# Kernel tuning notes

Measured on AMD Instinct MI355X. Metric: run time of the kernel, lower is better.

## Reference

```python
import jax, jax.numpy as jnp
import numpy as np
from math import sqrt

V, D, H, HD, L, F, P, NL = 32000, 768, 12, 64, 12, 3072, 2048, 2
B, S = 8, 1024
EPS = 1e-5


def setup_inputs() -> dict:
    key = jax.random.key(0)
    ks = jax.random.split(key, 12)
    n = lambda k, sh: (jax.random.normal(k, sh, jnp.float32) * 0.02)
    return {
        'tokens': jax.random.randint(ks[0], (B, S), 0, V, dtype=jnp.int32),
        'tok_emb': n(ks[1], (V, D)),
        'pos_emb': n(ks[2], (P, D)),
        'emb_ln_s': jnp.ones((D,), jnp.float32), 'emb_ln_b': jnp.zeros((D,), jnp.float32),
        'Wq': n(ks[3], (L, H, D, HD)), 'bq': jnp.zeros((L, H, HD), jnp.float32),
        'Wk': n(ks[4], (L, H, D, HD)), 'bk': jnp.zeros((L, H, HD), jnp.float32),
        'Wv': n(ks[5], (L, H, D, HD)), 'bv': jnp.zeros((L, H, HD), jnp.float32),
        'Wo': n(ks[6], (L, D, D)), 'bo': jnp.zeros((L, D), jnp.float32),
        'ln1_s': jnp.ones((L, D), jnp.float32), 'ln1_b': jnp.zeros((L, D), jnp.float32),
        'ln2_s': jnp.ones((L, D), jnp.float32), 'ln2_b': jnp.zeros((L, D), jnp.float32),
        'W1': n(ks[7], (L, D, F)), 'b1': jnp.zeros((L, F), jnp.float32),
        'W2': n(ks[8], (L, F, D)), 'b2': jnp.zeros((L, D), jnp.float32),
        'Wc': n(ks[9], (D, NL)), 'bc': jnp.zeros((NL,), jnp.float32),
    }


def _ln(x, s, b):
    m = jnp.mean(x, -1, keepdims=True)
    v = jnp.mean((x - m) ** 2, -1, keepdims=True)
    return (x - m) * jax.lax.rsqrt(v + EPS) * s + b


def reference(tokens, tok_emb, pos_emb, emb_ln_s, emb_ln_b,
              Wq, bq, Wk, bk, Wv, bv, Wo, bo,
              ln1_s, ln1_b, ln2_s, ln2_b, W1, b1, W2, b2, Wc, bc):
    b, s = tokens.shape
    # embeddings (dropout is eval-mode identity)
    x = tok_emb[tokens] + pos_emb[:s][None, :, :]          # [b, s, D]
    x = _ln(x, emb_ln_s, emb_ln_b)
    scale = 1.0 / sqrt(HD)
    for l in range(L):
        xn = _ln(x, ln1_s[l], ln1_b[l])
        q = jnp.einsum('bsd,hdk->bhsk', xn, Wq[l]) + bq[l][:, None, :]
        k = jnp.einsum('bsd,hdk->bhsk', xn, Wk[l]) + bk[l][:, None, :]
        v = jnp.einsum('bsd,hdk->bhsk', xn, Wv[l]) + bv[l][:, None, :]
        scores = jnp.einsum('bhsk,bhtk->bhst', q, k) * scale   # [b,H,s,s]
        w = jax.nn.softmax(scores, axis=-1)
        o = jnp.einsum('bhst,bhtk->bhsk', w, v)                # [b,H,s,HD]
        o = o.transpose(0, 2, 1, 3).reshape(b, s, D)           # concat heads
        x = x + o @ Wo[l] + bo[l]
        xn = _ln(x, ln2_s[l], ln2_b[l])
        h = jax.nn.gelu(xn @ W1[l] + b1[l], approximate=False)
        x = x + h @ W2[l] + b2[l]
    # CLS token -> classifier (dropout identity)
    return x[:, 0, :] @ Wc + bc                                # [b, NL]
```

## Files before the change

### kernel.cpp

```cpp
#include <hip/hip_runtime.h>
#include <hip/hip_bf16.h>
#include <math.h>

#define B_   8
#define S_   1024
#define D_   768
#define H_   12
#define HD_  64
#define L_   12
#define F_   3072
#define NTOK 8192

typedef __bf16 bf16x8 __attribute__((ext_vector_type(8)));
typedef float  f32x4  __attribute__((ext_vector_type(4)));
typedef unsigned short u16;

static __device__ __forceinline__ unsigned short f2bf_bits(float f) {
    __hip_bfloat16 h = __float2bfloat16(f);
    return __builtin_bit_cast(unsigned short, h);
}
static __device__ __forceinline__ float bf2f(unsigned short u) {
    unsigned int t = ((unsigned int)u) << 16;
    return __builtin_bit_cast(float, t);
}
static __device__ __forceinline__ void gload16(const void* g, void* l) {
    __builtin_amdgcn_global_load_lds(
        (__attribute__((address_space(1))) void*)g,
        (__attribute__((address_space(3))) void*)l, 16, 0, 0);
}

__global__ __launch_bounds__(256)
void prep_layer_kernel(const float* __restrict__ Wq, const float* __restrict__ Wk,
                       const float* __restrict__ Wv, const float* __restrict__ Wo,
                       const float* __restrict__ W1, const float* __restrict__ W2,
                       int l, __hip_bfloat16* __restrict__ wbuf)
{
    const int id = blockIdx.x;
    const float* src; __hip_bfloat16* dst;
    int R, C, r0, c0;
    if (id < 432) {
        int dtile = id % 12, t = id / 12;
        int which = t / 12, h = t % 12;
        src = (which == 0 ? Wq : which == 1 ? Wk : Wv) + (size_t)(l*12 + h) * 768 * 64;
        dst = wbuf + (size_t)(which*768 + h*64) * 768;
        R = 768; C = 64; r0 = dtile * 64; c0 = 0;
    } else if (id < 576) {
        int t = id - 432;
        src = Wo + (size_t)l * 768 * 768;
        dst = wbuf + 1769472;
        R = 768; C = 768; r0 = (t / 12) * 64; c0 = (t % 12) * 64;
    } else if (id < 1152) {
        int t = id - 576;
        src = W1 + (size_t)l * 768 * 3072;
        dst = wbuf + 2359296;
        R = 768; C = 3072; r0 = (t % 12) * 64; c0 = (t / 12) * 64;
    } else {
        int t = id - 1152;
        src = W2 + (size_t)l * 3072 * 768;
        dst = wbuf + 4718592;
        R = 3072; C = 768; r0 = (t / 12) * 64; c0 = (t % 12) * 64;
    }
    __shared__ float tile[64][65];
    for (int i = threadIdx.x; i < 4096; i += 256) {
        int rr = i >> 6, cc = i & 63;
        tile[rr][cc] = src[(size_t)(r0 + rr) * C + (c0 + cc)];
    }
    __syncthreads();
    for (int i = threadIdx.x; i < 4096; i += 256) {
        int cc = i >> 6, rr = i & 63;
        dst[(size_t)(c0 + cc) * R + (r0 + rr)] = __float2bfloat16(tile[rr][cc]);
    }
}

__global__ __launch_bounds__(256)
void prep_bqkv_kernel(const float* __restrict__ bq, const float* __restrict__ bk,
                      const float* __restrict__ bv, float* __restrict__ bqkv)
{
    int i = blockIdx.x * 256 + threadIdx.x;
    int l = i / 2304, c = i % 2304;
    int which = c / 768, hk = c % 768;
    const float* src = which == 0 ? bq : which == 1 ? bk : bv;
    bqkv[i] = src[l*768 + hk];
}

__global__ __launch_bounds__(256)
void embed_ln_kernel(const int* __restrict__ tokens, const float* __restrict__ tok_emb,
                     const float* __restrict__ pos_emb, const float* __restrict__ gam,
                     const float* __restrict__ bet, float* __restrict__ x)
{
    const int row  = blockIdx.x*4 + (threadIdx.x >> 6);
    const int lane = threadIdx.x & 63;
    const int s    = row & (S_-1);
    const int tok  = tokens[row];
    const float* te = tok_emb + (size_t)tok * D_;
    const float* pe = pos_emb + (size_t)s   * D_;
    float v[12]; float s1 = 0.f, s2 = 0.f;
#pragma unroll
    for (int c = 0; c < 3; ++c) {
        const int base = c*256 + lane*4;
        float4 a = *(const float4*)(te + base);
        float4 p = *(const float4*)(pe + base);
        float t0 = a.x+p.x, t1 = a.y+p.y, t2 = a.z+p.z, t3 = a.w+p.w;
        v[c*4+0]=t0; v[c*4+1]=t1; v[c*4+2]=t2; v[c*4+3]=t3;
        s1 += t0+t1+t2+t3;
        s2 += t0*t0 + t1*t1 + t2*t2 + t3*t3;
    }
#pragma unroll
    for (int off = 32; off > 0; off >>= 1) { s1 += __shfl_xor(s1, off); s2 += __shfl_xor(s2, off); }
    const float mean = s1 * (1.f/768.f);
    const float rstd = rsqrtf(s2*(1.f/768.f) - mean*mean + 1e-5f);
    float* xr = x + (size_t)row * D_;
#pragma unroll
    for (int c = 0; c < 3; ++c) {
        const int base = c*256 + lane*4;
        float4 g = *(const float4*)(gam + base);
        float4 bb = *(const float4*)(bet + base);
        float4 o;
        o.x = (v[c*4+0]-mean)*rstd*g.x + bb.x;
        o.y = (v[c*4+1]-mean)*rstd*g.y + bb.y;
        o.z = (v[c*4+2]-mean)*rstd*g.z + bb.z;
        o.w = (v[c*4+3]-mean)*rstd*g.w + bb.w;
        *(float4*)(xr + base) = o;
    }
}

__global__ __launch_bounds__(256)
void ln_kernel(const float* __restrict__ xin, const float* __restrict__ gam,
               const float* __restrict__ bet, __hip_bfloat16* __restrict__ out)
{
    const int row  = blockIdx.x*4 + (threadIdx.x >> 6);
    const int lane = threadIdx.x & 63;
    const float* xr = xin + (size_t)row * D_;
    float v[12]; float s1 = 0.f, s2 = 0.f;
#pragma unroll
    for (int c = 0; c < 3; ++c) {
        float4 t = *(const float4*)(xr + c*256 + lane*4);
        v[c*4+0]=t.x; v[c*4+1]=t.y; v[c*4+2]=t.z; v[c*4+3]=t.w;
        s1 += t.x+t.y+t.z+t.w;
        s2 += t.x*t.x + t.y*t.y + t.z*t.z + t.w*t.w;
    }
#pragma unroll
    for (int off = 32; off > 0; off >>= 1) { s1 += __shfl_xor(s1, off); s2 += __shfl_xor(s2, off); }
    const float mean = s1 * (1.f/768.f);
    const float rstd = rsqrtf(s2*(1.f/768.f) - mean*mean + 1e-5f);
    unsigned short* op = (unsigned short*)out + (size_t)row * D_;
#pragma unroll
    for (int c = 0; c < 3; ++c) {
        const int base = c*256 + lane*4;
        float4 g = *(const float4*)(gam + base);
        float4 bb = *(const float4*)(bet + base);
        ushort4 pk;
        pk.x = f2bf_bits((v[c*4+0]-mean)*rstd*g.x + bb.x);
        pk.y = f2bf_bits((v[c*4+1]-mean)*rstd*g.y + bb.y);
        pk.z = f2bf_bits((v[c*4+2]-mean)*rstd*g.z + bb.z);
        pk.w = f2bf_bits((v[c*4+3]-mean)*rstd*g.w + bb.w);
        *(ushort4*)(op + base) = pk;
    }
}

template<int EPI>
__global__ __launch_bounds__(256)
void gemm_kernel(const __hip_bfloat16* __restrict__ A,
                 const __hip_bfloat16* __restrict__ Bt,
                 const float* __restrict__ bias,
                 __hip_bfloat16* __restrict__ outb,
                 __hip_bfloat16* __restrict__ outv,
                 float* __restrict__ outf,
                 int M, int N, int K, int nTiles)
{
    __shared__ __hip_bfloat16 As[128*64];
    __shared__ __hip_bfloat16 Bs[128*64];

    const int tid  = threadIdx.x;
    const int lane = tid & 63;
    const int wid  = tid >> 6;

    const int nwg   = gridDim.x;
    const int chunk = nwg >> 3;
    const int bid   = blockIdx.x;
    const int swz   = (bid & 7) * chunk + (bid >> 3);
    const int m0 = (swz / nTiles) * 128;
    const int n0 = (swz % nTiles) * 128;

    const int srow = wid*32 + (lane >> 3);
    const int scol = ((lane & 7) ^ (srow & 7)) * 8;
    const __hip_bfloat16* aSrc = A  + (size_t)(m0 + srow) * K + scol;
    const __hip_bfloat16* bSrc = Bt + (size_t)(n0 + srow) * K + scol;
    char* aDst = (char*)As + wid*4096 + lane*16;
    char* bDst = (char*)Bs + wid*4096 + lane*16;

    f32x4 acc[4][4] = {};
    const int wm = wid >> 1, wn = wid & 1;
    const int cl = lane & 15, hi = lane >> 4;

    for (int kt = 0; kt < K; kt += 64) {
        __syncthreads();
#pragma unroll
        for (int i = 0; i < 4; ++i)
            gload16(aSrc + kt + (size_t)i*8*K, aDst + i*1024);
#pragma unroll
        for (int i = 0; i < 4; ++i)
            gload16(bSrc + kt + (size_t)i*8*K, bDst + i*1024);
        __syncthreads();

#pragma unroll
        for (int kk = 0; kk < 2; ++kk) {
            bf16x8 af[4], bfr[4];
#pragma unroll
            for (int m = 0; m < 4; ++m) {
                int row  = wm*64 + m*16 + cl;
                int slot = ((kk<<2) + hi) ^ (row & 7);
                af[m] = *(const bf16x8*)((const char*)As + row*128 + slot*16);
            }
#pragma unroll
            for (int n = 0; n < 4; ++n) {
                int row  = wn*64 + n*16 + cl;
                int slot = ((kk<<2) + hi) ^ (row & 7);
                bfr[n] = *(const bf16x8*)((const char*)Bs + row*128 + slot*16);
            }
#pragma unroll
            for (int m = 0; m < 4; ++m)
#pragma unroll
                for (int n = 0; n < 4; ++n)
                    acc[m][n] = __builtin_amdgcn_mfma_f32_16x16x32_bf16(af[m], bfr[n], acc[m][n], 0, 0, 0);
        }
    }

    const int rowBase = m0 + wm*64;
    const int colBase = n0 + wn*64;

    if constexpr (EPI == 0) {
        if (n0 < 1536) {
#pragma unroll
            for (int n = 0; n < 4; ++n) {
                const int col = colBase + n*16 + cl;
                const float bv = bias[col];
#pragma unroll
                for (int m = 0; m < 4; ++m) {
#pragma unroll
                    for (int i = 0; i < 4; ++i) {
                        const int row = rowBase + m*16 + hi*4 + i;
                        outb[(size_t)row*1536 + col] = __float2bfloat16(acc[m][n][i] + bv);
                    }
                }
            }
        } else {
#pragma unroll
            for (int n = 0; n < 4; ++n) {
                const int col = colBase + n*16 + cl;
                const float bv = bias[col];
                const int hd = col - 1536;
                u16* vrow = (u16*)outv + (size_t)hd * 1024;
#pragma unroll
                for (int m = 0; m < 4; ++m) {
                    const int row0 = rowBase + m*16 + hi*4;
                    const int b = row0 >> 10, s0 = row0 & 1023;
                    ushort4 pk;
                    pk.x = f2bf_bits(acc[m][n][0] + bv);
                    pk.y = f2bf_bits(acc[m][n][1] + bv);
                    pk.z = f2bf_bits(acc[m][n][2] + bv);
                    pk.w = f2bf_bits(acc[m][n][3] + bv);
                    *(ushort4*)(vrow + (size_t)b*12*64*1024 + s0) = pk;
                }
            }
        }
    } else {
#pragma unroll
        for (int n = 0; n < 4; ++n) {
            const int col = colBase + n*16 + cl;
            const float bv = bias[col];
#pragma unroll
            for (int m = 0; m < 4; ++m) {
#pragma unroll
                for (int i = 0; i < 4; ++i) {
                    const int row = rowBase + m*16 + hi*4 + i;
                    float v = acc[m][n][i] + bv;
                    if constexpr (EPI == 1) {
                        float g = 0.5f * v * (1.0f + erff(v * 0.70710678118f));
                        outb[(size_t)row*N + col] = __float2bfloat16(g);
                    } else {
                        outf[(size_t)row*N + col] += v;
                    }
                }
            }
        }
    }
    (void)M;
}

__global__ __launch_bounds__(256)
void attn_kernel(const __hip_bfloat16* __restrict__ qkb, const __hip_bfloat16* __restrict__ vtb,
                 __hip_bfloat16* __restrict__ attno)
{
    __shared__ __align__(16) char Ks[2][8192];
    __shared__ __align__(16) char Vs[2][8192];
    __shared__ __align__(16) char Ps[8192];

    const u16* qk = (const u16*)qkb;
    const u16* vt = (const u16*)vtb;
    const int nwg = gridDim.x, bid = blockIdx.x, chunk = nwg >> 3;
    const int swz = (bid & 7) * chunk + (bid >> 3);
    const int bh = swz >> 4, qb = swz & 15;
    const int b = bh / H_, h = bh % H_;
    const int tid = threadIdx.x;
    const int lane = tid & 63, wid = tid >> 6;
    const int cl = lane & 15, hi = lane >> 4;
    const size_t browq = (size_t)(b*S_ + qb*64);

    bf16x8 qf[2];
    {
        const u16* qp = qk + (browq + wid*16 + cl)*1536 + h*64;
        qf[0] = *(const bf16x8*)(qp + hi*8);
        qf[1] = *(const bf16x8*)(qp + 32 + hi*8);
    }

    const int lrow = lane >> 3;
    const int scol = ((lane & 7) ^ lrow) * 8;
    const u16* kbase = qk + ((size_t)b*S_ + wid*16 + lrow)*1536 + 768 + h*64 + scol;
    const u16* vbase = vt + (((size_t)(b*H_ + h))*64 + wid*16 + lrow)*1024 + scol;
    const int ldst = wid*2048 + lane*16;

    f32x4 acc_o[4] = {};
    float m_run = -1e30f;
    float l_part[4] = {0.f, 0.f, 0.f, 0.f};
    char* pbase = Ps + wid*2048;

    {
        gload16(kbase,                 Ks[0] + ldst);
        gload16(kbase + (size_t)8*1536, Ks[0] + ldst + 1024);
        gload16(vbase,                 Vs[0] + ldst);
        gload16(vbase + 8*1024,        Vs[0] + ldst + 1024);
    }

    for (int t = 0; t < 16; ++t) {
        __syncthreads();
        if (t < 15) {
            const int nb = (t+1) & 1;
            const u16* kn = kbase + (size_t)(t+1)*64*1536;
            const u16* vn = vbase + (t+1)*64;
            gload16(kn,                  Ks[nb] + ldst);
            gload16(kn + (size_t)8*1536, Ks[nb] + ldst + 1024);
            gload16(vn,                  Vs[nb] + ldst);
            gload16(vn + 8*1024,         Vs[nb] + ldst + 1024);
        }
        const char* ks = Ks[t & 1];
        const char* vs = Vs[t & 1];

        f32x4 sc[4] = {};
#pragma unroll
        for (int kk = 0; kk < 2; ++kk) {
            bf16x8 kf[4];
#pragma unroll
            for (int n = 0; n < 4; ++n) {
                const int row = n*16 + cl;
                kf[n] = *(const bf16x8*)(ks + row*128 + (((kk*4 + hi) ^ (cl & 7)) << 4));
            }
#pragma unroll
            for (int n = 0; n < 4; ++n)
                sc[n] = __builtin_amdgcn_mfma_f32_16x16x32_bf16(qf[kk], kf[n], sc[n], 0, 0, 0);
        }

#pragma unroll
        for (int n = 0; n < 4; ++n)
#pragma unroll
            for (int i = 0; i < 4; ++i)
                sc[n][i] *= 0.125f;

        float gmax = sc[0][0];
#pragma unroll
        for (int n = 0; n < 4; ++n)
#pragma unroll
            for (int i = 0; i < 4; ++i)
                gmax = fmaxf(gmax, sc[n][i]);
        gmax = fmaxf(gmax, __shfl_xor(gmax, 1));
        gmax = fmaxf(gmax, __shfl_xor(gmax, 2));
        gmax = fmaxf(gmax, __shfl_xor(gmax, 4));
        gmax = fmaxf(gmax, __shfl_xor(gmax, 8));
        if (gmax > m_run + 4.0f) {
            const float corr = __expf(m_run - gmax);
            m_run = gmax;
#pragma unroll
            for (int i = 0; i < 4; ++i) l_part[i] *= corr;
#pragma unroll
            for (int nd = 0; nd < 4; ++nd)
#pragma unroll
                for (int i = 0; i < 4; ++i)
                    acc_o[nd][i] *= corr;
        }

#pragma unroll
        for (int n = 0; n < 4; ++n) {
#pragma unroll
            for (int i = 0; i < 4; ++i) {
                const float e = __expf(sc[n][i] - m_run);
                l_part[i] += e;
                const int q = hi*4 + i;
                const int slot = (n*2 + (cl >> 3)) ^ (q & 7);
                *(u16*)(pbase + q*128 + slot*16 + (cl & 7)*2) = f2bf_bits(e);
            }
        }

        asm volatile("s_waitcnt lgkmcnt(0)" ::: "memory");
        __builtin_amdgcn_sched_barrier(0);

#pragma unroll
        for (int kk = 0; kk < 2; ++kk) {
            const bf16x8 pf = *(const bf16x8*)(pbase + cl*128 + (((kk*4 + hi) ^ (cl & 7)) << 4));
            bf16x8 vf[4];
#pragma unroll
            for (int nd = 0; nd < 4; ++nd) {
                const int d = nd*16 + cl;
                vf[nd] = *(const bf16x8*)(vs + d*128 + (((kk*4 + hi) ^ (d & 7)) << 4));
            }
#pragma unroll
            for (int nd = 0; nd < 4; ++nd)
                acc_o[nd] = __builtin_amdgcn_mfma_f32_16x16x32_bf16(pf, vf[nd], acc_o[nd], 0, 0, 0);
        }
    }

    u16* op = (u16*)attno;
#pragma unroll
    for (int i = 0; i < 4; ++i) {
        float l = l_part[i];
        l += __shfl_xor(l, 1);
        l += __shfl_xor(l, 2);
        l += __shfl_xor(l, 4);
        l += __shfl_xor(l, 8);
        const float inv = 1.f / l;
        const size_t row = browq + wid*16 + hi*4 + i;
#pragma unroll
        for (int nd = 0; nd < 4; ++nd)
            op[row*768 + h*64 + nd*16 + cl] = f2bf_bits(acc_o[nd][i] * inv);
    }
}

__global__ __launch_bounds__(256)
void cls_kernel(const float* __restrict__ x, const float* __restrict__ Wc,
                const float* __restrict__ bc, float* __restrict__ out)
{
    const int b = blockIdx.x;
    const float* xr = x + (size_t)b * S_ * D_;
    float a0 = 0.f, a1 = 0.f;
    for (int d = threadIdx.x; d < 768; d += 256) {
        float xv = xr[d];
        a0 += xv * Wc[d*2+0];
        a1 += xv * Wc[d*2+1];
    }
#pragma unroll
    for (int off = 32; off > 0; off >>= 1) { a0 += __shfl_xor(a0, off); a1 += __shfl_xor(a1, off); }
    __shared__ float r0[4], r1[4];
    const int w = threadIdx.x >> 6;
    if ((threadIdx.x & 63) == 0) { r0[w] = a0; r1[w] = a1; }
    __syncthreads();
    if (threadIdx.x == 0) {
        out[b*2+0] = r0[0]+r0[1]+r0[2]+r0[3] + bc[0];
        out[b*2+1] = r1[0]+r1[1]+r1[2]+r1[3] + bc[1];
    }
}

extern "C" void kernel_launch(void* const* d_in, const int* in_sizes, int n_in,
                              void* d_out, int out_size, void* d_ws, size_t ws_size,
                              hipStream_t stream)
{
    const int*   tokens  = (const int*)  d_in[0];
    const float* tok_emb = (const float*)d_in[1];
    const float* pos_emb = (const float*)d_in[2];
    const float* e_s     = (const float*)d_in[3];
    const float* e_b     = (const float*)d_in[4];
    const float* Wq      = (const float*)d_in[5];
    const float* bq      = (const float*)d_in[6];
    const float* Wk      = (const float*)d_in[7];
    const float* bk      = (const float*)d_in[8];
    const float* Wv      = (const float*)d_in[9];
    const float* bv      = (const float*)d_in[10];
    const float* Wo      = (const float*)d_in[11];
    const float* bo      = (const float*)d_in[12];
    const float* l1s     = (const float*)d_in[13];
    const float* l1b     = (const float*)d_in[14];
    const float* l2s     = (const float*)d_in[15];
    const float* l2b     = (const float*)d_in[16];
    const float* W1      = (const float*)d_in[17];
    const float* b1      = (const float*)d_in[18];
    const float* W2      = (const float*)d_in[19];
    const float* b2      = (const float*)d_in[20];
    const float* Wc      = (const float*)d_in[21];
    const float* bc      = (const float*)d_in[22];
    (void)in_sizes; (void)n_in; (void)out_size;

    if (ws_size < 102346752) return;

    char* ws = (char*)d_ws;
    __hip_bfloat16* wbuf = (__hip_bfloat16*)(ws + 0);
    float*          bqkv = (float*)(ws + 14155776);
    float*          x    = (float*)(ws + 14266368);
    __hip_bfloat16* xn   = (__hip_bfloat16*)(ws + 39432192);
    __hip_bfloat16* qk   = (__hip_bfloat16*)(ws + 52015104);
    __hip_bfloat16* vT   = (__hip_bfloat16*)(ws + 77180928);
    __hip_bfloat16* att  = (__hip_bfloat16*)(ws + 89763840);
    __hip_bfloat16* hbuf = qk;

    __hip_bfloat16* wqkv_t = wbuf;
    __hip_bfloat16* wo_t   = wbuf + 1769472;
    __hip_bfloat16* w1_t   = wbuf + 2359296;
    __hip_bfloat16* w2_t   = wbuf + 4718592;

    prep_bqkv_kernel<<<108, 256, 0, stream>>>(bq, bk, bv, bqkv);
    embed_ln_kernel<<<2048, 256, 0, stream>>>(tokens, tok_emb, pos_emb, e_s, e_b, x);

    for (int l = 0; l < L_; ++l) {
        prep_layer_kernel<<<1728, 256, 0, stream>>>(Wq, Wk, Wv, Wo, W1, W2, l, wbuf);
        ln_kernel<<<2048, 256, 0, stream>>>(x, l1s + l*768, l1b + l*768, xn);
        gemm_kernel<0><<<1152, 256, 0, stream>>>(xn, wqkv_t, bqkv + l*2304, qk, vT, nullptr, NTOK, 2304, 768, 18);
        attn_kernel<<<1536, 256, 0, stream>>>(qk, vT, att);
        gemm_kernel<2><<<384, 256, 0, stream>>>(att, wo_t, bo + l*768, nullptr, nullptr, x, NTOK, 768, 768, 6);
        ln_kernel<<<2048, 256, 0, stream>>>(x, l2s + l*768, l2b + l*768, xn);
        gemm_kernel<1><<<1536, 256, 0, stream>>>(xn, w1_t, b1 + l*3072, hbuf, nullptr, nullptr, NTOK, 3072, 768, 24);
        gemm_kernel<2><<<384, 256, 0, stream>>>(hbuf, w2_t, b2 + l*768, nullptr, nullptr, x, NTOK, 768, 3072, 6);
    }
    cls_kernel<<<8, 256, 0, stream>>>(x, Wc, bc, (float*)d_out);
}
```

Before: 3.598 ms.

## Use 64-row tiles for residual GEMMs, separate V transpose, tanh GELU

Adds a 64x128-tile GEMM kernel for the N=768 residual projections so twice as many workgroups fill the GPU. The transposed V store in the QKV epilogue is replaced by a row-major store plus a separate LDS transpose kernel. The erf-based GELU is replaced by a tanh approximation computed with exp. These trade an extra kernel launch and V round-trip, plus a small numerical deviation from exact GELU, for better occupancy and cheaper epilogues.

```diff
diff --git a/kernel.cpp b/kernel.cpp
--- a/kernel.cpp
+++ b/kernel.cpp
@@ -165,8 +165,7 @@
                  const float* __restrict__ bias,
                  __hip_bfloat16* __restrict__ outb,
                  __hip_bfloat16* __restrict__ outv,
-                 float* __restrict__ outf,
-                 int M, int N, int K, int nTiles)
+                 int N, int K, int nTiles)
 {
     __shared__ __hip_bfloat16 As[128*64];
     __shared__ __hip_bfloat16 Bs[128*64];
@@ -250,17 +249,13 @@
                 const int col = colBase + n*16 + cl;
                 const float bv = bias[col];
                 const int hd = col - 1536;
-                u16* vrow = (u16*)outv + (size_t)hd * 1024;
 #pragma unroll
                 for (int m = 0; m < 4; ++m) {
-                    const int row0 = rowBase + m*16 + hi*4;
-                    const int b = row0 >> 10, s0 = row0 & 1023;
-                    ushort4 pk;
-                    pk.x = f2bf_bits(acc[m][n][0] + bv);
-                    pk.y = f2bf_bits(acc[m][n][1] + bv);
-                    pk.z = f2bf_bits(acc[m][n][2] + bv);
-                    pk.w = f2bf_bits(acc[m][n][3] + bv);
-                    *(ushort4*)(vrow + (size_t)b*12*64*1024 + s0) = pk;
+#pragma unroll
+                    for (int i = 0; i < 4; ++i) {
+                        const int row = rowBase + m*16 + hi*4 + i;
+                        outv[(size_t)row*768 + hd] = __float2bfloat16(acc[m][n][i] + bv);
+                    }
                 }
             }
         }
@@ -274,18 +269,118 @@
 #pragma unroll
                 for (int i = 0; i < 4; ++i) {
                     const int row = rowBase + m*16 + hi*4 + i;
-                    float v = acc[m][n][i] + bv;
-                    if constexpr (EPI == 1) {
-                        float g = 0.5f * v * (1.0f + erff(v * 0.70710678118f));
-                        outb[(size_t)row*N + col] = __float2bfloat16(g);
-                    } else {
-                        outf[(size_t)row*N + col] += v;
-                    }
+                    const float v = acc[m][n][i] + bv;
+                    const float y = 0.7978845608f * (v + 0.044715f*v*v*v);
+                    const float e = __expf(-2.0f * fabsf(y));
+                    const float th = (1.0f - e) / (1.0f + e);
+                    const float g = 0.5f * v * (1.0f + copysignf(th, y));
+                    outb[(size_t)row*N + col] = __float2bfloat16(g);
                 }
             }
         }
     }
-    (void)M;
+}
+
+__global__ __launch_bounds__(256)
+void gemm64_res_kernel(const __hip_bfloat16* __restrict__ A,
+                       const __hip_bfloat16* __restrict__ Bt,
+                       const float* __restrict__ bias,
+                       float* __restrict__ outf,
+                       int N, int K, int nTiles)
+{
+    __shared__ __hip_bfloat16 As[64*64];
+    __shared__ __hip_bfloat16 Bs[128*64];
+
+    const int tid  = threadIdx.x;
+    const int lane = tid & 63;
+    const int wid  = tid >> 6;
+
+    const int nwg   = gridDim.x;
+    const int chunk = nwg >> 3;
+    const int bid   = blockIdx.x;
+    const int swz   = (bid & 7) * chunk + (bid >> 3);
+    const int m0 = (swz / nTiles) * 64;
+    const int n0 = (swz % nTiles) * 128;
+
+    const int lrow = lane >> 3;
+    const int scol = ((lane & 7) ^ lrow) * 8;
+    const __hip_bfloat16* aSrc = A  + (size_t)(m0 + wid*16 + lrow) * K + scol;
+    const __hip_bfloat16* bSrc = Bt + (size_t)(n0 + wid*32 + lrow) * K + scol;
+    char* aDst = (char*)As + wid*2048 + lane*16;
+    char* bDst = (char*)Bs + wid*4096 + lane*16;
+
+    f32x4 acc[2][4] = {};
+    const int wm = wid >> 1, wn = wid & 1;
+    const int cl = lane & 15, hi = lane >> 4;
+
+    for (int kt = 0; kt < K; kt += 64) {
+        __syncthreads();
+#pragma unroll
+        for (int i = 0; i < 2; ++i)
+            gload16(aSrc + kt + (size_t)i*8*K, aDst + i*1024);
+#pragma unroll
+        for (int i = 0; i < 4; ++i)
+            gload16(bSrc + kt + (size_t)i*8*K, bDst + i*1024);
+        __syncthreads();
+
+#pragma unroll
+        for (int kk = 0; kk < 2; ++kk) {
+            bf16x8 af[2], bfr[4];
+#pragma unroll
+            for (int m = 0; m < 2; ++m) {
+                int row  = wm*32 + m*16 + cl;
+                int slot = ((kk<<2) + hi) ^ (row & 7);
+                af[m] = *(const bf16x8*)((const char*)As + row*128 + slot*16);
+            }
+#pragma unroll
+            for (int n = 0; n < 4; ++n) {
+                int row  = wn*64 + n*16 + cl;
+                int slot = ((kk<<2) + hi) ^ (row & 7);
+                bfr[n] = *(const bf16x8*)((const char*)Bs + row*128 + slot*16);
+            }
+#pragma unroll
+            for (int m = 0; m < 2; ++m)
+#pragma unroll
+                for (int n = 0; n < 4; ++n)
+                    acc[m][n] = __builtin_amdgcn_mfma_f32_16x16x32_bf16(af[m], bfr[n], acc[m][n], 0, 0, 0);
+        }
+    }
+
+    const int rowBase = m0 + wm*32;
+    const int colBase = n0 + wn*64;
+#pragma unroll
+    for (int n = 0; n < 4; ++n) {
+        const int col = colBase + n*16 + cl;
+        const float bv = bias[col];
+#pragma unroll
+        for (int m = 0; m < 2; ++m) {
+#pragma unroll
+            for (int i = 0; i < 4; ++i) {
+                const int row = rowBase + m*16 + hi*4 + i;
+                outf[(size_t)row*N + col] += acc[m][n][i] + bv;
+            }
+        }
+    }
+}
+
+__global__ __launch_bounds__(256)
+void vtrans_kernel(const __hip_bfloat16* __restrict__ vp, __hip_bfloat16* __restrict__ vT)
+{
+    __shared__ u16 tile[64][65];
+    const int id = blockIdx.x;
+    const int b = id / 192, r = id % 192;
+    const int hdt = r / 16, st = r % 16;
+    const u16* src = (const u16*)vp + ((size_t)(b*1024 + st*64))*768 + hdt*64;
+    u16* dst = (u16*)vT + ((size_t)(b*768 + hdt*64))*1024 + st*64;
+    for (int i = threadIdx.x; i < 4096; i += 256) {
+        int rr = i >> 6, cc = i & 63;
+        tile[rr][cc] = src[(size_t)rr*768 + cc];
+    }
+    __syncthreads();
+    for (int i = threadIdx.x; i < 4096; i += 256) {
+        int cc = i >> 6, rr = i & 63;
+        dst[(size_t)cc*1024 + rr] = tile[rr][cc];
+    }
 }
 
 __global__ __launch_bounds__(256)
@@ -326,10 +421,10 @@
     char* pbase = Ps + wid*2048;
 
     {
-        gload16(kbase,                 Ks[0] + ldst);
+        gload16(kbase,                  Ks[0] + ldst);
         gload16(kbase + (size_t)8*1536, Ks[0] + ldst + 1024);
-        gload16(vbase,                 Vs[0] + ldst);
-        gload16(vbase + 8*1024,        Vs[0] + ldst + 1024);
+        gload16(vbase,                  Vs[0] + ldst);
+        gload16(vbase + 8*1024,         Vs[0] + ldst + 1024);
     }
 
     for (int t = 0; t < 16; ++t) {
@@ -497,6 +592,7 @@
     __hip_bfloat16* qk   = (__hip_bfloat16*)(ws + 52015104);
     __hip_bfloat16* vT   = (__hip_bfloat16*)(ws + 77180928);
     __hip_bfloat16* att  = (__hip_bfloat16*)(ws + 89763840);
+    __hip_bfloat16* vpl  = att;
     __hip_bfloat16* hbuf = qk;
 
     __hip_bfloat16* wqkv_t = wbuf;
@@ -510,12 +606,13 @@
     for (int l = 0; l < L_; ++l) {
         prep_layer_kernel<<<1728, 256, 0, stream>>>(Wq, Wk, Wv, Wo, W1, W2, l, wbuf);
         ln_kernel<<<2048, 256, 0, stream>>>(x, l1s + l*768, l1b + l*768, xn);
-        gemm_kernel<0><<<1152, 256, 0, stream>>>(xn, wqkv_t, bqkv + l*2304, qk, vT, nullptr, NTOK, 2304, 768, 18);
+        gemm_kernel<0><<<1152, 256, 0, stream>>>(xn, wqkv_t, bqkv + l*2304, qk, vpl, 2304, 768, 18);
+        vtrans_kernel<<<1536, 256, 0, stream>>>(vpl, vT);
         attn_kernel<<<1536, 256, 0, stream>>>(qk, vT, att);
-        gemm_kernel<2><<<384, 256, 0, stream>>>(att, wo_t, bo + l*768, nullptr, nullptr, x, NTOK, 768, 768, 6);
+        gemm64_res_kernel<<<768, 256, 0, stream>>>(att, wo_t, bo + l*768, x, 768, 768, 6);
         ln_kernel<<<2048, 256, 0, stream>>>(x, l2s + l*768, l2b + l*768, xn);
-        gemm_kernel<1><<<1536, 256, 0, stream>>>(xn, w1_t, b1 + l*3072, hbuf, nullptr, nullptr, NTOK, 3072, 768, 24);
-        gemm_kernel<2><<<384, 256, 0, stream>>>(hbuf, w2_t, b2 + l*768, nullptr, nullptr, x, NTOK, 768, 3072, 6);
+        gemm_kernel<1><<<1536, 256, 0, stream>>>(xn, w1_t, b1 + l*3072, hbuf, nullptr, 3072, 768, 24);
+        gemm64_res_kernel<<<768, 256, 0, stream>>>(hbuf, w2_t, b2 + l*768, x, 768, 3072, 6);
     }
     cls_kernel<<<8, 256, 0, stream>>>(x, Wc, bc, (float*)d_out);
 }
```

Result: faster. 3.363 ms (-6.5%).
